# Optimization experiments

Measured on AMD Instinct MI355X. Metric: run time of the kernel, lower is better.

## Reference

```python
import jax, jax.numpy as jnp
import numpy as np

L = 2    # num_graph_layers
T = 16   # num_tasks (batch of episodes)
N = 128  # num_samples (nodes per episode)
F = 128  # num_node_feats
BN_EPS = 1e-5


def setup_inputs() -> dict:
    key = jax.random.key(0)
    ks = jax.random.split(key, 8)
    return {
        "node_feats": jax.random.normal(ks[0], (T, N, F), dtype=jnp.float32),
        "edge_feats": jax.random.uniform(ks[1], (T, N, N, F), dtype=jnp.float32),
        # Conv3d(3->1, 1x1x1) weight+bias per layer -> 3 scalars + 1 bias
        "edge_w": (jax.random.normal(ks[2], (L, 3), dtype=jnp.float32) * 0.5),
        "edge_b": (jax.random.normal(ks[3], (L,), dtype=jnp.float32) * 0.1),
        # Conv2d(2->1, 1x1, no bias) -> 2 scalars per layer
        "comb_w": (jax.random.normal(ks[4], (L, 2), dtype=jnp.float32) * 0.5),
        # Conv1d(F->F, k=1, no bias) -> [out,in] per layer
        "node_w": (jax.random.normal(ks[5], (L, F, F), dtype=jnp.float32) / np.sqrt(F).astype(np.float32)),
        # BatchNorm1d affine params
        "bn_gamma": jnp.ones((L, F), dtype=jnp.float32),
        "bn_beta": jnp.zeros((L, F), dtype=jnp.float32),
    }


def _lrelu(x):
    return jnp.where(x >= 0, x, 0.01 * x)  # torch LeakyReLU default slope


def _sim_cal(x):
    # x: [T,N,F] -> clamped [cos_sim, 1-cos_sim]: [T,2,N,N]
    g = jnp.einsum('tnf,tmf->tnm', x, x)
    nrm = jnp.linalg.norm(x, axis=-1)              # [T,N]
    denom = nrm[:, :, None] * nrm[:, None, :] + 1e-6
    sim = (g / denom)[:, None]                     # [T,1,N,N]
    pred = jnp.concatenate([sim, 1.0 - sim], axis=1)
    return jnp.clip(pred, 0.0, 1.0)


def reference(node_feats, edge_feats, edge_w, edge_b, comb_w, node_w, bn_gamma, bn_beta):
    outs = [_sim_cal(node_feats)]
    n = node_feats.shape[1]
    diag_mask = (1.0 - jnp.eye(n, dtype=node_feats.dtype))[None, :, :, None]  # [1,N,N,1]
    for l in range(L):
        x = node_feats                                     # [T,N,F]
        # --- EdgeUpdateNetwork: Conv3d(3->1,1x1x1) over channels [x_i, x_i-x_j, edge] + tanh ---
        diff = x[:, :, None, :] - x[:, None, :, :]         # [T,N,N,F]
        xi = jnp.broadcast_to(x[:, :, None, :], diff.shape)
        e = jnp.tanh(edge_w[l, 0] * xi + edge_w[l, 1] * diff
                     + edge_w[l, 2] * edge_feats + edge_b[l])
        edge_feats = e * diag_mask                         # zero diagonal
        # --- NodeUpdateNetwork ---
        aggr = edge_feats.sum(axis=2)                      # [T,N,F]
        h = _lrelu(comb_w[l, 0] * x + comb_w[l, 1] * aggr) # Conv2d(2->1) + LeakyReLU
        y = jnp.einsum('tnf,gf->tng', h, node_w[l])        # Conv1d(F->F, k=1)
        mu = y.mean(axis=(0, 1))                           # BN over (batch, length)
        var = y.var(axis=(0, 1))
        y = (y - mu) * jax.lax.rsqrt(var + BN_EPS) * bn_gamma[l] + bn_beta[l]
        node_feats = _lrelu(y)
        outs.append(_sim_cal(node_feats))
    return tuple(outs)
```

## Files before the change

### kernel.cpp

```cpp
#include <hip/hip_runtime.h>

#define T_ 16
#define N_ 128
#define F_ 128

__device__ __forceinline__ float fast_tanh(float x) {
    float e = __expf(2.0f * x);
    return 1.0f - __fdividef(2.0f, e + 1.0f);
}

__device__ __forceinline__ float lrelu(float v) {
    return v >= 0.0f ? v : 0.01f * v;
}

__global__ void wprep(const float* __restrict__ W, float* __restrict__ WT,
                      float* __restrict__ bn) {
    int l = blockIdx.y;
    int idx = blockIdx.x * 256 + threadIdx.x;
    int g = idx >> 7, f = idx & 127;
    WT[l * 16384 + f * 128 + g] = W[l * 16384 + idx];
    if (l == 0 && blockIdx.x == 0) {
        bn[threadIdx.x] = 0.0f;
        bn[256 + threadIdx.x] = 0.0f;
    }
}

template<int LAYER>
__global__ __launch_bounds__(256) void edge_k(const float* __restrict__ x0,
                                              const float* __restrict__ x1,
                                              const float* __restrict__ E,
                                              const float* __restrict__ ew,
                                              const float* __restrict__ eb,
                                              float* __restrict__ aggrP) {
    __shared__ float4 red[256];
    int b = blockIdx.x;
    int ti = b >> 2, q = b & 3;
    int t = ti >> 7, i = ti & 127;
    int tid = threadIdx.x, jl = tid >> 5, fg = tid & 31;

    const float4* xt0 = (const float4*)(x0 + (size_t)t * 16384);
    const float4* xt1 = (const float4*)(x1 + (size_t)t * 16384);
    const float4* Ei  = (const float4*)(E + (size_t)ti * 16384);

    float w02 = ew[2], b0 = eb[0];
    float c0 = ew[0] + ew[1], nw01 = -ew[1];
    float c1 = 0.f, nw11 = 0.f, w12 = 0.f, b1 = 0.f;
    if constexpr (LAYER == 1) { c1 = ew[3] + ew[4]; nw11 = -ew[4]; w12 = ew[5]; b1 = eb[1]; }

    float4 xi0 = xt0[i * 32 + fg];
    float4 xi1 = xi0;
    if constexpr (LAYER == 1) xi1 = xt1[i * 32 + fg];

    float4 a = make_float4(0.f, 0.f, 0.f, 0.f);
    int jbase = q * 32;

    float4 xj0[4], ev[4], xj1[4];
    #pragma unroll
    for (int k = 0; k < 4; ++k) {
        int j = jbase + k * 8 + jl;
        ev[k]  = Ei[j * 32 + fg];
        xj0[k] = xt0[j * 32 + fg];
        if constexpr (LAYER == 1) xj1[k] = xt1[j * 32 + fg];
    }

    #pragma unroll
    for (int k = 0; k < 4; ++k) {
        int j = jbase + k * 8 + jl;
        float msk = (j != i) ? 1.0f : 0.0f;
        if constexpr (LAYER == 0) {
            a.x += msk * fast_tanh(fmaf(c0, xi0.x, fmaf(w02, ev[k].x, fmaf(nw01, xj0[k].x, b0))));
            a.y += msk * fast_tanh(fmaf(c0, xi0.y, fmaf(w02, ev[k].y, fmaf(nw01, xj0[k].y, b0))));
            a.z += msk * fast_tanh(fmaf(c0, xi0.z, fmaf(w02, ev[k].z, fmaf(nw01, xj0[k].z, b0))));
            a.w += msk * fast_tanh(fmaf(c0, xi0.w, fmaf(w02, ev[k].w, fmaf(nw01, xj0[k].w, b0))));
        } else {
            float e0x = fast_tanh(fmaf(c0, xi0.x, fmaf(w02, ev[k].x, fmaf(nw01, xj0[k].x, b0))));
            float e0y = fast_tanh(fmaf(c0, xi0.y, fmaf(w02, ev[k].y, fmaf(nw01, xj0[k].y, b0))));
            float e0z = fast_tanh(fmaf(c0, xi0.z, fmaf(w02, ev[k].z, fmaf(nw01, xj0[k].z, b0))));
            float e0w = fast_tanh(fmaf(c0, xi0.w, fmaf(w02, ev[k].w, fmaf(nw01, xj0[k].w, b0))));
            a.x += msk * fast_tanh(fmaf(c1, xi1.x, fmaf(w12, e0x, fmaf(nw11, xj1[k].x, b1))));
            a.y += msk * fast_tanh(fmaf(c1, xi1.y, fmaf(w12, e0y, fmaf(nw11, xj1[k].y, b1))));
            a.z += msk * fast_tanh(fmaf(c1, xi1.z, fmaf(w12, e0z, fmaf(nw11, xj1[k].z, b1))));
            a.w += msk * fast_tanh(fmaf(c1, xi1.w, fmaf(w12, e0w, fmaf(nw11, xj1[k].w, b1))));
        }
    }

    red[tid] = a;
    __syncthreads();
    if (tid < 32) {
        float4 r = red[tid];
        #pragma unroll
        for (int k = 1; k < 8; ++k) {
            float4 o = red[tid + 32 * k];
            r.x += o.x; r.y += o.y; r.z += o.z; r.w += o.w;
        }
        ((float4*)(aggrP + (size_t)q * 262144))[ti * 32 + tid] = r;
    }
}

__global__ __launch_bounds__(128) void node_k(const float* __restrict__ x,
                                              const float* __restrict__ aggrP,
                                              const float* __restrict__ cw,
                                              const float* __restrict__ WT,
                                              float* __restrict__ y_out,
                                              float* __restrict__ bnL) {
    __shared__ float hs[8][128];
    int t = blockIdx.x, ch = blockIdx.y, g = threadIdx.x;
    float c0 = cw[0], c1 = cw[1];
    size_t base = ((size_t)t * 128 + ch * 8) * 128;
    #pragma unroll
    for (int r = 0; r < 8; ++r) {
        float xv = x[base + r * 128 + g];
        float av = aggrP[base + r * 128 + g]
                 + aggrP[262144 + base + r * 128 + g]
                 + aggrP[524288 + base + r * 128 + g]
                 + aggrP[786432 + base + r * 128 + g];
        hs[r][g] = lrelu(fmaf(c0, xv, c1 * av));
    }
    __syncthreads();
    float acc[8];
    #pragma unroll
    for (int r = 0; r < 8; ++r) acc[r] = 0.0f;
    #pragma unroll 4
    for (int f = 0; f < 128; ++f) {
        float wv = WT[f * 128 + g];
        #pragma unroll
        for (int r = 0; r < 8; ++r) acc[r] = fmaf(hs[r][f], wv, acc[r]);
    }
    float s = 0.0f, ss = 0.0f;
    #pragma unroll
    for (int r = 0; r < 8; ++r) {
        y_out[base + r * 128 + g] = acc[r];
        s += acc[r];
        ss += acc[r] * acc[r];
    }
    atomicAdd(&bnL[g], s);
    atomicAdd(&bnL[128 + g], ss);
}

template<bool BN>
__global__ __launch_bounds__(256) void sim_k(const float* __restrict__ x,
                                             const float* __restrict__ bnS,
                                             const float* __restrict__ gamma,
                                             const float* __restrict__ beta,
                                             float* __restrict__ out,
                                             float* __restrict__ xout) {
    __shared__ float Xs[128][132];
    __shared__ float nrm[128];
    int t = blockIdx.x, ch = blockIdx.y;
    int tid = threadIdx.x;
    int m = tid & 127, rh = tid >> 7;
    const float* xt = x + (size_t)t * (N_ * F_);
    int fg = (tid & 31) * 4, ko = tid >> 5;

    float4 sc, sh;
    if constexpr (BN) {
        float4 s1 = *(const float4*)(bnS + fg);
        float4 s2 = *(const float4*)(bnS + 128 + fg);
        float4 ga = *(const float4*)(gamma + fg);
        float4 be = *(const float4*)(beta + fg);
        const float inv_n = 1.0f / 2048.0f;
        float mx = s1.x * inv_n, my = s1.y * inv_n, mz = s1.z * inv_n, mw = s1.w * inv_n;
        sc.x = rsqrtf(s2.x * inv_n - mx * mx + 1e-5f) * ga.x;
        sc.y = rsqrtf(s2.y * inv_n - my * my + 1e-5f) * ga.y;
        sc.z = rsqrtf(s2.z * inv_n - mz * mz + 1e-5f) * ga.z;
        sc.w = rsqrtf(s2.w * inv_n - mw * mw + 1e-5f) * ga.w;
        sh.x = be.x - mx * sc.x;
        sh.y = be.y - my * sc.y;
        sh.z = be.z - mz * sc.z;
        sh.w = be.w - mw * sc.w;
    }

    bool wout = false;
    if constexpr (BN) wout = (blockIdx.y == 0) && (xout != nullptr);
    for (int kb = 0; kb < 128; kb += 8) {
        int k = kb + ko;
        float4 v = *(const float4*)(xt + k * 128 + fg);
        if constexpr (BN) {
            v.x = lrelu(fmaf(v.x, sc.x, sh.x));
            v.y = lrelu(fmaf(v.y, sc.y, sh.y));
            v.z = lrelu(fmaf(v.z, sc.z, sh.z));
            v.w = lrelu(fmaf(v.w, sc.w, sh.w));
            if (wout) *(float4*)(xout + (size_t)t * 16384 + k * 128 + fg) = v;
        }
        *(float4*)&Xs[k][fg] = v;
    }
    __syncthreads();

    if (tid < 128) {
        float s = 0.0f;
        #pragma unroll 8
        for (int f = 0; f < 128; f += 4) {
            float4 v = *(float4*)&Xs[m][f];
            s += v.x * v.x + v.y * v.y + v.z * v.z + v.w * v.w;
        }
        nrm[m] = sqrtf(s);
    }
    __syncthreads();

    float acc[4];
    #pragma unroll
    for (int r = 0; r < 4; ++r) acc[r] = 0.0f;

    for (int fc = 0; fc < 128; fc += 32) {
        float xm[32];
        #pragma unroll
        for (int f = 0; f < 32; f += 4) {
            float4 v = *(float4*)&Xs[m][fc + f];
            xm[f] = v.x; xm[f + 1] = v.y; xm[f + 2] = v.z; xm[f + 3] = v.w;
        }
        #pragma unroll
        for (int r = 0; r < 4; ++r) {
            int n = ch * 8 + rh * 4 + r;
            #pragma unroll
            for (int f = 0; f < 32; f += 4) {
                float4 v = *(float4*)&Xs[n][fc + f];
                acc[r] = fmaf(xm[f], v.x,
                         fmaf(xm[f + 1], v.y,
                         fmaf(xm[f + 2], v.z,
                         fmaf(xm[f + 3], v.w, acc[r]))));
            }
        }
    }

    float nm = nrm[m];
    size_t ob = (size_t)t * 2 * 16384;
    #pragma unroll
    for (int r = 0; r < 4; ++r) {
        int n = ch * 8 + rh * 4 + r;
        float denom = nrm[n] * nm + 1e-6f;
        float sim = __fdividef(acc[r], denom);
        float s0 = fminf(fmaxf(sim, 0.0f), 1.0f);
        float s1 = fminf(fmaxf(1.0f - sim, 0.0f), 1.0f);
        out[ob + (size_t)n * 128 + m] = s0;
        out[ob + 16384 + (size_t)n * 128 + m] = s1;
    }
}

extern "C" void kernel_launch(void* const* d_in, const int* in_sizes, int n_in,
                              void* d_out, int out_size, void* d_ws, size_t ws_size,
                              hipStream_t stream) {
    const float* x0    = (const float*)d_in[0];
    const float* E     = (const float*)d_in[1];
    const float* ew    = (const float*)d_in[2];
    const float* eb    = (const float*)d_in[3];
    const float* cw    = (const float*)d_in[4];
    const float* nw    = (const float*)d_in[5];
    const float* gamma = (const float*)d_in[6];
    const float* beta  = (const float*)d_in[7];
    float* out = (float*)d_out;

    float* ws    = (float*)d_ws;
    float* x1    = ws;
    float* yb    = ws + 262144;
    float* aggrP = ws + 524288;
    float* bn    = ws + 1572864;
    float* WT    = ws + 1573376;

    wprep<<<dim3(64, 2), 256, 0, stream>>>(nw, WT, bn);

    sim_k<false><<<dim3(16, 16), 256, 0, stream>>>(x0, nullptr, nullptr, nullptr, out, nullptr);

    edge_k<0><<<8192, 256, 0, stream>>>(x0, x0, E, ew, eb, aggrP);
    node_k<<<dim3(16, 16), 128, 0, stream>>>(x0, aggrP, cw, WT, yb, bn);
    sim_k<true><<<dim3(16, 16), 256, 0, stream>>>(yb, bn, gamma, beta, out + 524288, x1);

    edge_k<1><<<8192, 256, 0, stream>>>(x0, x1, E, ew, eb, aggrP);
    node_k<<<dim3(16, 16), 128, 0, stream>>>(x1, aggrP, cw + 2, WT + 16384, yb, bn + 256);
    sim_k<true><<<dim3(16, 16), 256, 0, stream>>>(yb, bn + 256, gamma + 128, beta + 128,
                                                  out + 1048576, nullptr);
}
```

Before: 303.1 us.

## Fuse node update and similarity via cooperative grid sync; merge weight prep

```diff
diff --git a/kernel.cpp b/kernel.cpp
--- a/kernel.cpp
+++ b/kernel.cpp
@@ -1,4 +1,7 @@
 #include <hip/hip_runtime.h>
+#include <hip/hip_cooperative_groups.h>
+
+namespace cg = cooperative_groups;
 
 #define T_ 16
 #define N_ 128
@@ -13,15 +16,84 @@
     return v >= 0.0f ? v : 0.01f * v;
 }
 
-__global__ void wprep(const float* __restrict__ W, float* __restrict__ WT,
-                      float* __restrict__ bn) {
-    int l = blockIdx.y;
-    int idx = blockIdx.x * 256 + threadIdx.x;
-    int g = idx >> 7, f = idx & 127;
-    WT[l * 16384 + f * 128 + g] = W[l * 16384 + idx];
-    if (l == 0 && blockIdx.x == 0) {
-        bn[threadIdx.x] = 0.0f;
-        bn[256 + threadIdx.x] = 0.0f;
+__global__ __launch_bounds__(256) void sim0_prep_k(const float* __restrict__ x,
+                                                   const float* __restrict__ W,
+                                                   float* __restrict__ WT,
+                                                   float* __restrict__ bn,
+                                                   float* __restrict__ out) {
+    __shared__ float Xs[128][132];
+    __shared__ float nrm[128];
+    int tid = threadIdx.x;
+
+    if (blockIdx.y == 16) {
+        int idx4 = blockIdx.x * 256 + tid;
+        #pragma unroll
+        for (int k = 0; k < 8; ++k) {
+            int lin = k * 4096 + idx4;
+            int l = lin >> 14, idx = lin & 16383;
+            int g = idx >> 7, f = idx & 127;
+            WT[l * 16384 + f * 128 + g] = W[lin];
+        }
+        if (blockIdx.x == 0) { bn[tid] = 0.0f; bn[256 + tid] = 0.0f; }
+        return;
+    }
+
+    int t = blockIdx.x, ch = blockIdx.y;
+    int m = tid & 127, rh = tid >> 7;
+    const float* xt = x + (size_t)t * (N_ * F_);
+    int fg = (tid & 31) * 4, ko = tid >> 5;
+
+    for (int kb = 0; kb < 128; kb += 8) {
+        int k = kb + ko;
+        *(float4*)&Xs[k][fg] = *(const float4*)(xt + k * 128 + fg);
+    }
+    __syncthreads();
+
+    if (tid < 128) {
+        float s = 0.0f;
+        #pragma unroll 8
+        for (int f = 0; f < 128; f += 4) {
+            float4 v = *(float4*)&Xs[m][f];
+            s += v.x * v.x + v.y * v.y + v.z * v.z + v.w * v.w;
+        }
+        nrm[m] = sqrtf(s);
+    }
+    __syncthreads();
+
+    float acc[4];
+    #pragma unroll
+    for (int r = 0; r < 4; ++r) acc[r] = 0.0f;
+
+    for (int fc = 0; fc < 128; fc += 32) {
+        float xm[32];
+        #pragma unroll
+        for (int f = 0; f < 32; f += 4) {
+            float4 v = *(float4*)&Xs[m][fc + f];
+            xm[f] = v.x; xm[f + 1] = v.y; xm[f + 2] = v.z; xm[f + 3] = v.w;
+        }
+        #pragma unroll
+        for (int r = 0; r < 4; ++r) {
+            int n = ch * 8 + rh * 4 + r;
+            #pragma unroll
+            for (int f = 0; f < 32; f += 4) {
+                float4 v = *(float4*)&Xs[n][fc + f];
+                acc[r] = fmaf(xm[f], v.x,
+                         fmaf(xm[f + 1], v.y,
+                         fmaf(xm[f + 2], v.z,
+                         fmaf(xm[f + 3], v.w, acc[r]))));
+            }
+        }
+    }
+
+    float nm = nrm[m];
+    size_t ob = (size_t)t * 2 * 16384;
+    #pragma unroll
+    for (int r = 0; r < 4; ++r) {
+        int n = ch * 8 + rh * 4 + r;
+        float denom = nrm[n] * nm + 1e-6f;
+        float sim = __fdividef(acc[r], denom);
+        out[ob + (size_t)n * 128 + m] = fminf(fmaxf(sim, 0.0f), 1.0f);
+        out[ob + 16384 + (size_t)n * 128 + m] = fminf(fmaxf(1.0f - sim, 0.0f), 1.0f);
     }
 }
 
@@ -97,65 +169,78 @@
     }
 }
 
-__global__ __launch_bounds__(128) void node_k(const float* __restrict__ x,
-                                              const float* __restrict__ aggrP,
-                                              const float* __restrict__ cw,
-                                              const float* __restrict__ WT,
-                                              float* __restrict__ y_out,
-                                              float* __restrict__ bnL) {
-    __shared__ float hs[8][128];
-    int t = blockIdx.x, ch = blockIdx.y, g = threadIdx.x;
-    float c0 = cw[0], c1 = cw[1];
-    size_t base = ((size_t)t * 128 + ch * 8) * 128;
-    #pragma unroll
-    for (int r = 0; r < 8; ++r) {
-        float xv = x[base + r * 128 + g];
-        float av = aggrP[base + r * 128 + g]
-                 + aggrP[262144 + base + r * 128 + g]
-                 + aggrP[524288 + base + r * 128 + g]
-                 + aggrP[786432 + base + r * 128 + g];
-        hs[r][g] = lrelu(fmaf(c0, xv, c1 * av));
-    }
-    __syncthreads();
-    float acc[8];
-    #pragma unroll
-    for (int r = 0; r < 8; ++r) acc[r] = 0.0f;
-    #pragma unroll 4
-    for (int f = 0; f < 128; ++f) {
-        float wv = WT[f * 128 + g];
-        #pragma unroll
-        for (int r = 0; r < 8; ++r) acc[r] = fmaf(hs[r][f], wv, acc[r]);
-    }
-    float s = 0.0f, ss = 0.0f;
-    #pragma unroll
-    for (int r = 0; r < 8; ++r) {
-        y_out[base + r * 128 + g] = acc[r];
-        s += acc[r];
-        ss += acc[r] * acc[r];
-    }
-    atomicAdd(&bnL[g], s);
-    atomicAdd(&bnL[128 + g], ss);
-}
-
-template<bool BN>
-__global__ __launch_bounds__(256) void sim_k(const float* __restrict__ x,
-                                             const float* __restrict__ bnS,
-                                             const float* __restrict__ gamma,
-                                             const float* __restrict__ beta,
-                                             float* __restrict__ out,
-                                             float* __restrict__ xout) {
-    __shared__ float Xs[128][132];
-    __shared__ float nrm[128];
+union NodeSimShared {
+    struct { float hs[8][128]; float ya[8][128]; } n;
+    struct { float Xs[128][132]; float nrm[128]; } s;
+};
+
+template<bool WRITE_X>
+__global__ __launch_bounds__(256) void node_sim_k(const float* __restrict__ x,
+                                                  const float* __restrict__ aggrP,
+                                                  const float* __restrict__ cw,
+                                                  const float* __restrict__ WT,
+                                                  float* __restrict__ yb,
+                                                  float* __restrict__ bnL,
+                                                  const float* __restrict__ gamma,
+                                                  const float* __restrict__ beta,
+                                                  float* __restrict__ out,
+                                                  float* __restrict__ xout) {
+    __shared__ NodeSimShared sm;
     int t = blockIdx.x, ch = blockIdx.y;
     int tid = threadIdx.x;
-    int m = tid & 127, rh = tid >> 7;
-    const float* xt = x + (size_t)t * (N_ * F_);
+    int g = tid & 127, half = tid >> 7;
+    size_t base = ((size_t)t * 128 + ch * 8) * 128;
+
+    {
+        float c0 = cw[0], c1 = cw[1];
+        #pragma unroll
+        for (int rr = 0; rr < 4; ++rr) {
+            int r = half * 4 + rr;
+            size_t o = base + (size_t)r * 128 + g;
+            float xv = x[o];
+            float av = aggrP[o] + aggrP[262144 + o] + aggrP[524288 + o] + aggrP[786432 + o];
+            sm.n.hs[r][g] = lrelu(fmaf(c0, xv, c1 * av));
+        }
+        __syncthreads();
+        float acc[8];
+        #pragma unroll
+        for (int r = 0; r < 8; ++r) acc[r] = 0.0f;
+        const float* wp = WT + (size_t)(half * 64) * 128 + g;
+        #pragma unroll 4
+        for (int f = 0; f < 64; ++f) {
+            float wv = wp[(size_t)f * 128];
+            #pragma unroll
+            for (int r = 0; r < 8; ++r) acc[r] = fmaf(sm.n.hs[r][half * 64 + f], wv, acc[r]);
+        }
+        if (half) {
+            #pragma unroll
+            for (int r = 0; r < 8; ++r) sm.n.ya[r][g] = acc[r];
+        }
+        __syncthreads();
+        if (!half) {
+            float s = 0.0f, ss = 0.0f;
+            #pragma unroll
+            for (int r = 0; r < 8; ++r) {
+                float y = acc[r] + sm.n.ya[r][g];
+                yb[base + (size_t)r * 128 + g] = y;
+                s += y;
+                ss += y * y;
+            }
+            atomicAdd(&bnL[g], s);
+            atomicAdd(&bnL[128 + g], ss);
+        }
+    }
+
+    cg::this_grid().sync();
+
+    int m = g, rh = half;
+    const float* xt = yb + (size_t)t * (N_ * F_);
     int fg = (tid & 31) * 4, ko = tid >> 5;
 
     float4 sc, sh;
-    if constexpr (BN) {
-        float4 s1 = *(const float4*)(bnS + fg);
-        float4 s2 = *(const float4*)(bnS + 128 + fg);
+    {
+        float4 s1 = *(const float4*)(bnL + fg);
+        float4 s2 = *(const float4*)(bnL + 128 + fg);
         float4 ga = *(const float4*)(gamma + fg);
         float4 be = *(const float4*)(beta + fg);
         const float inv_n = 1.0f / 2048.0f;
@@ -170,19 +255,16 @@
         sh.w = be.w - mw * sc.w;
     }
 
-    bool wout = false;
-    if constexpr (BN) wout = (blockIdx.y == 0) && (xout != nullptr);
+    bool wout = WRITE_X && (ch == 0);
     for (int kb = 0; kb < 128; kb += 8) {
         int k = kb + ko;
         float4 v = *(const float4*)(xt + k * 128 + fg);
-        if constexpr (BN) {
-            v.x = lrelu(fmaf(v.x, sc.x, sh.x));
-            v.y = lrelu(fmaf(v.y, sc.y, sh.y));
-            v.z = lrelu(fmaf(v.z, sc.z, sh.z));
-            v.w = lrelu(fmaf(v.w, sc.w, sh.w));
-            if (wout) *(float4*)(xout + (size_t)t * 16384 + k * 128 + fg) = v;
-        }
-        *(float4*)&Xs[k][fg] = v;
+        v.x = lrelu(fmaf(v.x, sc.x, sh.x));
+        v.y = lrelu(fmaf(v.y, sc.y, sh.y));
+        v.z = lrelu(fmaf(v.z, sc.z, sh.z));
+        v.w = lrelu(fmaf(v.w, sc.w, sh.w));
+        if (wout) *(float4*)(xout + (size_t)t * 16384 + k * 128 + fg) = v;
+        *(float4*)&sm.s.Xs[k][fg] = v;
     }
     __syncthreads();
 
@@ -190,10 +272,10 @@
         float s = 0.0f;
         #pragma unroll 8
         for (int f = 0; f < 128; f += 4) {
-            float4 v = *(float4*)&Xs[m][f];
+            float4 v = *(float4*)&sm.s.Xs[m][f];
             s += v.x * v.x + v.y * v.y + v.z * v.z + v.w * v.w;
         }
-        nrm[m] = sqrtf(s);
+        sm.s.nrm[m] = sqrtf(s);
     }
     __syncthreads();
 
@@ -205,7 +287,7 @@
         float xm[32];
         #pragma unroll
         for (int f = 0; f < 32; f += 4) {
-            float4 v = *(float4*)&Xs[m][fc + f];
+            float4 v = *(float4*)&sm.s.Xs[m][fc + f];
             xm[f] = v.x; xm[f + 1] = v.y; xm[f + 2] = v.z; xm[f + 3] = v.w;
         }
         #pragma unroll
@@ -213,7 +295,7 @@
             int n = ch * 8 + rh * 4 + r;
             #pragma unroll
             for (int f = 0; f < 32; f += 4) {
-                float4 v = *(float4*)&Xs[n][fc + f];
+                float4 v = *(float4*)&sm.s.Xs[n][fc + f];
                 acc[r] = fmaf(xm[f], v.x,
                          fmaf(xm[f + 1], v.y,
                          fmaf(xm[f + 2], v.z,
@@ -222,17 +304,15 @@
         }
     }
 
-    float nm = nrm[m];
+    float nm = sm.s.nrm[m];
     size_t ob = (size_t)t * 2 * 16384;
     #pragma unroll
     for (int r = 0; r < 4; ++r) {
         int n = ch * 8 + rh * 4 + r;
-        float denom = nrm[n] * nm + 1e-6f;
+        float denom = sm.s.nrm[n] * nm + 1e-6f;
         float sim = __fdividef(acc[r], denom);
-        float s0 = fminf(fmaxf(sim, 0.0f), 1.0f);
-        float s1 = fminf(fmaxf(1.0f - sim, 0.0f), 1.0f);
-        out[ob + (size_t)n * 128 + m] = s0;
-        out[ob + 16384 + (size_t)n * 128 + m] = s1;
+        out[ob + (size_t)n * 128 + m] = fminf(fmaxf(sim, 0.0f), 1.0f);
+        out[ob + 16384 + (size_t)n * 128 + m] = fminf(fmaxf(1.0f - sim, 0.0f), 1.0f);
     }
 }
 
@@ -256,16 +336,31 @@
     float* bn    = ws + 1572864;
     float* WT    = ws + 1573376;
 
-    wprep<<<dim3(64, 2), 256, 0, stream>>>(nw, WT, bn);
-
-    sim_k<false><<<dim3(16, 16), 256, 0, stream>>>(x0, nullptr, nullptr, nullptr, out, nullptr);
+    sim0_prep_k<<<dim3(16, 17), 256, 0, stream>>>(x0, nw, WT, bn, out);
 
     edge_k<0><<<8192, 256, 0, stream>>>(x0, x0, E, ew, eb, aggrP);
-    node_k<<<dim3(16, 16), 128, 0, stream>>>(x0, aggrP, cw, WT, yb, bn);
-    sim_k<true><<<dim3(16, 16), 256, 0, stream>>>(yb, bn, gamma, beta, out + 524288, x1);
+
+    {
+        const float* xa = x0; const float* ap = aggrP; const float* cwp = cw;
+        const float* wt = WT; float* ybp = yb; float* bnp = bn;
+        const float* ga = gamma; const float* be = beta;
+        float* op = out + 524288; float* xo = x1;
+        void* args[] = {(void*)&xa, (void*)&ap, (void*)&cwp, (void*)&wt, (void*)&ybp,
+                        (void*)&bnp, (void*)&ga, (void*)&be, (void*)&op, (void*)&xo};
+        hipLaunchCooperativeKernel((const void*)node_sim_k<true>, dim3(16, 16),
+                                   dim3(256, 1, 1), args, 0, stream);
+    }
 
     edge_k<1><<<8192, 256, 0, stream>>>(x0, x1, E, ew, eb, aggrP);
-    node_k<<<dim3(16, 16), 128, 0, stream>>>(x1, aggrP, cw + 2, WT + 16384, yb, bn + 256);
-    sim_k<true><<<dim3(16, 16), 256, 0, stream>>>(yb, bn + 256, gamma + 128, beta + 128,
-                                                  out + 1048576, nullptr);
-}
+
+    {
+        const float* xa = x1; const float* ap = aggrP; const float* cwp = cw + 2;
+        const float* wt = WT + 16384; float* ybp = yb; float* bnp = bn + 256;
+        const float* ga = gamma + 128; const float* be = beta + 128;
+        float* op = out + 1048576; float* xo = nullptr;
+        void* args[] = {(void*)&xa, (void*)&ap, (void*)&cwp, (void*)&wt, (void*)&ybp,
+                        (void*)&bnp, (void*)&ga, (void*)&be, (void*)&op, (void*)&xo};
+        hipLaunchCooperativeKernel((const void*)node_sim_k<false>, dim3(16, 16),
+                                   dim3(256, 1, 1), args, 0, stream);
+    }
+}
```

Result: slower. 372.4 us (+22.9%).

## Merge weight prep, initial similarity and layer-0 edge update into one kernel

Applied to the files above, without the earlier changes.

```diff
diff --git a/kernel.cpp b/kernel.cpp
--- a/kernel.cpp
+++ b/kernel.cpp
@@ -13,25 +13,142 @@
     return v >= 0.0f ? v : 0.01f * v;
 }
 
-__global__ void wprep(const float* __restrict__ W, float* __restrict__ WT,
-                      float* __restrict__ bn) {
-    int l = blockIdx.y;
-    int idx = blockIdx.x * 256 + threadIdx.x;
-    int g = idx >> 7, f = idx & 127;
-    WT[l * 16384 + f * 128 + g] = W[l * 16384 + idx];
-    if (l == 0 && blockIdx.x == 0) {
-        bn[threadIdx.x] = 0.0f;
-        bn[256 + threadIdx.x] = 0.0f;
-    }
-}
-
-template<int LAYER>
-__global__ __launch_bounds__(256) void edge_k(const float* __restrict__ x0,
-                                              const float* __restrict__ x1,
-                                              const float* __restrict__ E,
-                                              const float* __restrict__ ew,
-                                              const float* __restrict__ eb,
-                                              float* __restrict__ aggrP) {
+union MergedShared {
+    float4 red[256];
+    struct { float Xs[128][36]; float nrm[128]; } s;
+};
+
+__global__ __launch_bounds__(256) void merged0_k(const float* __restrict__ x0,
+                                                 const float* __restrict__ E,
+                                                 const float* __restrict__ ew,
+                                                 const float* __restrict__ eb,
+                                                 const float* __restrict__ W,
+                                                 float* __restrict__ WT,
+                                                 float* __restrict__ bn,
+                                                 float* __restrict__ aggrP,
+                                                 float* __restrict__ out) {
+    __shared__ MergedShared sm;
+    int b = blockIdx.x;
+    int tid = threadIdx.x;
+
+    if (b < 256) {
+        int t = b >> 4, ch = b & 15;
+        int m = tid & 127, rh = tid >> 7;
+        const float* xt = x0 + (size_t)t * 16384;
+        float nacc = 0.0f;
+        float acc[4] = {0.f, 0.f, 0.f, 0.f};
+        for (int c = 0; c < 4; ++c) {
+            #pragma unroll
+            for (int qq = 0; qq < 4; ++qq) {
+                int q = tid * 4 + qq;
+                int k = q >> 3, f4 = q & 7;
+                *(float4*)&sm.s.Xs[k][f4 * 4] =
+                    *(const float4*)(xt + k * 128 + c * 32 + f4 * 4);
+            }
+            __syncthreads();
+            if (tid < 128) {
+                #pragma unroll
+                for (int f = 0; f < 32; f += 4) {
+                    float4 v = *(float4*)&sm.s.Xs[m][f];
+                    nacc += v.x * v.x + v.y * v.y + v.z * v.z + v.w * v.w;
+                }
+            }
+            #pragma unroll
+            for (int f = 0; f < 32; f += 4) {
+                float4 vm = *(float4*)&sm.s.Xs[m][f];
+                #pragma unroll
+                for (int r = 0; r < 4; ++r) {
+                    int n = ch * 8 + rh * 4 + r;
+                    float4 vn = *(float4*)&sm.s.Xs[n][f];
+                    acc[r] = fmaf(vm.x, vn.x,
+                             fmaf(vm.y, vn.y,
+                             fmaf(vm.z, vn.z,
+                             fmaf(vm.w, vn.w, acc[r]))));
+                }
+            }
+            __syncthreads();
+        }
+        if (tid < 128) sm.s.nrm[tid] = sqrtf(nacc);
+        __syncthreads();
+
+        float nm = sm.s.nrm[m];
+        size_t ob = (size_t)t * 2 * 16384;
+        #pragma unroll
+        for (int r = 0; r < 4; ++r) {
+            int n = ch * 8 + rh * 4 + r;
+            float denom = sm.s.nrm[n] * nm + 1e-6f;
+            float sim = __fdividef(acc[r], denom);
+            out[ob + (size_t)n * 128 + m] = fminf(fmaxf(sim, 0.0f), 1.0f);
+            out[ob + 16384 + (size_t)n * 128 + m] = fminf(fmaxf(1.0f - sim, 0.0f), 1.0f);
+        }
+        return;
+    }
+
+    if (b < 272) {
+        int idx4 = (b - 256) * 256 + tid;
+        #pragma unroll
+        for (int k = 0; k < 8; ++k) {
+            int lin = k * 4096 + idx4;
+            int l = lin >> 14, idx = lin & 16383;
+            int g = idx >> 7, f = idx & 127;
+            WT[l * 16384 + f * 128 + g] = W[lin];
+        }
+        if (idx4 < 512) bn[idx4] = 0.0f;
+        return;
+    }
+
+    int bb = b - 272;
+    int ti = bb >> 2, q = bb & 3;
+    int t = ti >> 7, i = ti & 127;
+    int jl = tid >> 5, fg = tid & 31;
+
+    const float4* xt0 = (const float4*)(x0 + (size_t)t * 16384);
+    const float4* Ei  = (const float4*)(E + (size_t)ti * 16384);
+
+    float w02 = ew[2], b0 = eb[0];
+    float c0 = ew[0] + ew[1], nw01 = -ew[1];
+
+    float4 xi0 = xt0[i * 32 + fg];
+    float4 a = make_float4(0.f, 0.f, 0.f, 0.f);
+    int jbase = q * 32;
+
+    float4 xj0[4], ev[4];
+    #pragma unroll
+    for (int k = 0; k < 4; ++k) {
+        int j = jbase + k * 8 + jl;
+        ev[k]  = Ei[j * 32 + fg];
+        xj0[k] = xt0[j * 32 + fg];
+    }
+
+    #pragma unroll
+    for (int k = 0; k < 4; ++k) {
+        int j = jbase + k * 8 + jl;
+        float msk = (j != i) ? 1.0f : 0.0f;
+        a.x += msk * fast_tanh(fmaf(c0, xi0.x, fmaf(w02, ev[k].x, fmaf(nw01, xj0[k].x, b0))));
+        a.y += msk * fast_tanh(fmaf(c0, xi0.y, fmaf(w02, ev[k].y, fmaf(nw01, xj0[k].y, b0))));
+        a.z += msk * fast_tanh(fmaf(c0, xi0.z, fmaf(w02, ev[k].z, fmaf(nw01, xj0[k].z, b0))));
+        a.w += msk * fast_tanh(fmaf(c0, xi0.w, fmaf(w02, ev[k].w, fmaf(nw01, xj0[k].w, b0))));
+    }
+
+    sm.red[tid] = a;
+    __syncthreads();
+    if (tid < 32) {
+        float4 r = sm.red[tid];
+        #pragma unroll
+        for (int k = 1; k < 8; ++k) {
+            float4 o = sm.red[tid + 32 * k];
+            r.x += o.x; r.y += o.y; r.z += o.z; r.w += o.w;
+        }
+        ((float4*)(aggrP + (size_t)q * 262144))[ti * 32 + tid] = r;
+    }
+}
+
+__global__ __launch_bounds__(256) void edge1_k(const float* __restrict__ x0,
+                                               const float* __restrict__ x1,
+                                               const float* __restrict__ E,
+                                               const float* __restrict__ ew,
+                                               const float* __restrict__ eb,
+                                               float* __restrict__ aggrP) {
     __shared__ float4 red[256];
     int b = blockIdx.x;
     int ti = b >> 2, q = b & 3;
@@ -44,12 +161,10 @@
 
     float w02 = ew[2], b0 = eb[0];
     float c0 = ew[0] + ew[1], nw01 = -ew[1];
-    float c1 = 0.f, nw11 = 0.f, w12 = 0.f, b1 = 0.f;
-    if constexpr (LAYER == 1) { c1 = ew[3] + ew[4]; nw11 = -ew[4]; w12 = ew[5]; b1 = eb[1]; }
+    float c1 = ew[3] + ew[4], nw11 = -ew[4], w12 = ew[5], b1 = eb[1];
 
     float4 xi0 = xt0[i * 32 + fg];
-    float4 xi1 = xi0;
-    if constexpr (LAYER == 1) xi1 = xt1[i * 32 + fg];
+    float4 xi1 = xt1[i * 32 + fg];
 
     float4 a = make_float4(0.f, 0.f, 0.f, 0.f);
     int jbase = q * 32;
@@ -60,28 +175,21 @@
         int j = jbase + k * 8 + jl;
         ev[k]  = Ei[j * 32 + fg];
         xj0[k] = xt0[j * 32 + fg];
-        if constexpr (LAYER == 1) xj1[k] = xt1[j * 32 + fg];
+        xj1[k] = xt1[j * 32 + fg];
     }
 
     #pragma unroll
     for (int k = 0; k < 4; ++k) {
         int j = jbase + k * 8 + jl;
         float msk = (j != i) ? 1.0f : 0.0f;
-        if constexpr (LAYER == 0) {
-            a.x += msk * fast_tanh(fmaf(c0, xi0.x, fmaf(w02, ev[k].x, fmaf(nw01, xj0[k].x, b0))));
-            a.y += msk * fast_tanh(fmaf(c0, xi0.y, fmaf(w02, ev[k].y, fmaf(nw01, xj0[k].y, b0))));
-            a.z += msk * fast_tanh(fmaf(c0, xi0.z, fmaf(w02, ev[k].z, fmaf(nw01, xj0[k].z, b0))));
-            a.w += msk * fast_tanh(fmaf(c0, xi0.w, fmaf(w02, ev[k].w, fmaf(nw01, xj0[k].w, b0))));
-        } else {
-            float e0x = fast_tanh(fmaf(c0, xi0.x, fmaf(w02, ev[k].x, fmaf(nw01, xj0[k].x, b0))));
-            float e0y = fast_tanh(fmaf(c0, xi0.y, fmaf(w02, ev[k].y, fmaf(nw01, xj0[k].y, b0))));
-            float e0z = fast_tanh(fmaf(c0, xi0.z, fmaf(w02, ev[k].z, fmaf(nw01, xj0[k].z, b0))));
-            float e0w = fast_tanh(fmaf(c0, xi0.w, fmaf(w02, ev[k].w, fmaf(nw01, xj0[k].w, b0))));
-            a.x += msk * fast_tanh(fmaf(c1, xi1.x, fmaf(w12, e0x, fmaf(nw11, xj1[k].x, b1))));
-            a.y += msk * fast_tanh(fmaf(c1, xi1.y, fmaf(w12, e0y, fmaf(nw11, xj1[k].y, b1))));
-            a.z += msk * fast_tanh(fmaf(c1, xi1.z, fmaf(w12, e0z, fmaf(nw11, xj1[k].z, b1))));
-            a.w += msk * fast_tanh(fmaf(c1, xi1.w, fmaf(w12, e0w, fmaf(nw11, xj1[k].w, b1))));
-        }
+        float e0x = fast_tanh(fmaf(c0, xi0.x, fmaf(w02, ev[k].x, fmaf(nw01, xj0[k].x, b0))));
+        float e0y = fast_tanh(fmaf(c0, xi0.y, fmaf(w02, ev[k].y, fmaf(nw01, xj0[k].y, b0))));
+        float e0z = fast_tanh(fmaf(c0, xi0.z, fmaf(w02, ev[k].z, fmaf(nw01, xj0[k].z, b0))));
+        float e0w = fast_tanh(fmaf(c0, xi0.w, fmaf(w02, ev[k].w, fmaf(nw01, xj0[k].w, b0))));
+        a.x += msk * fast_tanh(fmaf(c1, xi1.x, fmaf(w12, e0x, fmaf(nw11, xj1[k].x, b1))));
+        a.y += msk * fast_tanh(fmaf(c1, xi1.y, fmaf(w12, e0y, fmaf(nw11, xj1[k].y, b1))));
+        a.z += msk * fast_tanh(fmaf(c1, xi1.z, fmaf(w12, e0z, fmaf(nw11, xj1[k].z, b1))));
+        a.w += msk * fast_tanh(fmaf(c1, xi1.w, fmaf(w12, e0w, fmaf(nw11, xj1[k].w, b1))));
     }
 
     red[tid] = a;
@@ -137,23 +245,22 @@
     atomicAdd(&bnL[128 + g], ss);
 }
 
-template<bool BN>
-__global__ __launch_bounds__(256) void sim_k(const float* __restrict__ x,
-                                             const float* __restrict__ bnS,
-                                             const float* __restrict__ gamma,
-                                             const float* __restrict__ beta,
-                                             float* __restrict__ out,
-                                             float* __restrict__ xout) {
+__global__ __launch_bounds__(256) void simbn_k(const float* __restrict__ yb,
+                                               const float* __restrict__ bnS,
+                                               const float* __restrict__ gamma,
+                                               const float* __restrict__ beta,
+                                               float* __restrict__ out,
+                                               float* __restrict__ xout) {
     __shared__ float Xs[128][132];
     __shared__ float nrm[128];
     int t = blockIdx.x, ch = blockIdx.y;
     int tid = threadIdx.x;
     int m = tid & 127, rh = tid >> 7;
-    const float* xt = x + (size_t)t * (N_ * F_);
+    const float* xt = yb + (size_t)t * (N_ * F_);
     int fg = (tid & 31) * 4, ko = tid >> 5;
 
     float4 sc, sh;
-    if constexpr (BN) {
+    {
         float4 s1 = *(const float4*)(bnS + fg);
         float4 s2 = *(const float4*)(bnS + 128 + fg);
         float4 ga = *(const float4*)(gamma + fg);
@@ -170,18 +277,15 @@
         sh.w = be.w - mw * sc.w;
     }
 
-    bool wout = false;
-    if constexpr (BN) wout = (blockIdx.y == 0) && (xout != nullptr);
+    bool wout = (blockIdx.y == 0) && (xout != nullptr);
     for (int kb = 0; kb < 128; kb += 8) {
         int k = kb + ko;
         float4 v = *(const float4*)(xt + k * 128 + fg);
-        if constexpr (BN) {
-            v.x = lrelu(fmaf(v.x, sc.x, sh.x));
-            v.y = lrelu(fmaf(v.y, sc.y, sh.y));
-            v.z = lrelu(fmaf(v.z, sc.z, sh.z));
-            v.w = lrelu(fmaf(v.w, sc.w, sh.w));
-            if (wout) *(float4*)(xout + (size_t)t * 16384 + k * 128 + fg) = v;
-        }
+        v.x = lrelu(fmaf(v.x, sc.x, sh.x));
+        v.y = lrelu(fmaf(v.y, sc.y, sh.y));
+        v.z = lrelu(fmaf(v.z, sc.z, sh.z));
+        v.w = lrelu(fmaf(v.w, sc.w, sh.w));
+        if (wout) *(float4*)(xout + (size_t)t * 16384 + k * 128 + fg) = v;
         *(float4*)&Xs[k][fg] = v;
     }
     __syncthreads();
@@ -229,10 +333,8 @@
         int n = ch * 8 + rh * 4 + r;
         float denom = nrm[n] * nm + 1e-6f;
         float sim = __fdividef(acc[r], denom);
-        float s0 = fminf(fmaxf(sim, 0.0f), 1.0f);
-        float s1 = fminf(fmaxf(1.0f - sim, 0.0f), 1.0f);
-        out[ob + (size_t)n * 128 + m] = s0;
-        out[ob + 16384 + (size_t)n * 128 + m] = s1;
+        out[ob + (size_t)n * 128 + m] = fminf(fmaxf(sim, 0.0f), 1.0f);
+        out[ob + 16384 + (size_t)n * 128 + m] = fminf(fmaxf(1.0f - sim, 0.0f), 1.0f);
     }
 }
 
@@ -256,16 +358,16 @@
     float* bn    = ws + 1572864;
     float* WT    = ws + 1573376;
 
-    wprep<<<dim3(64, 2), 256, 0, stream>>>(nw, WT, bn);
-
-    sim_k<false><<<dim3(16, 16), 256, 0, stream>>>(x0, nullptr, nullptr, nullptr, out, nullptr);
-
-    edge_k<0><<<8192, 256, 0, stream>>>(x0, x0, E, ew, eb, aggrP);
+    merged0_k<<<8464, 256, 0, stream>>>(x0, E, ew, eb, nw, WT, bn, aggrP, out);
+
     node_k<<<dim3(16, 16), 128, 0, stream>>>(x0, aggrP, cw, WT, yb, bn);
-    sim_k<true><<<dim3(16, 16), 256, 0, stream>>>(yb, bn, gamma, beta, out + 524288, x1);
-
-    edge_k<1><<<8192, 256, 0, stream>>>(x0, x1, E, ew, eb, aggrP);
+
+    simbn_k<<<dim3(16, 16), 256, 0, stream>>>(yb, bn, gamma, beta, out + 524288, x1);
+
+    edge1_k<<<8192, 256, 0, stream>>>(x0, x1, E, ew, eb, aggrP);
+
     node_k<<<dim3(16, 16), 128, 0, stream>>>(x1, aggrP, cw + 2, WT + 16384, yb, bn + 256);
-    sim_k<true><<<dim3(16, 16), 256, 0, stream>>>(yb, bn + 256, gamma + 128, beta + 128,
-                                                  out + 1048576, nullptr);
-}
+
+    simbn_k<<<dim3(16, 16), 256, 0, stream>>>(yb, bn + 256, gamma + 128, beta + 128,
+                                              out + 1048576, nullptr);
+}
```

Result: faster. 297.0 us (-2.0%).
